# Kernel tuning notes

Hardware: AMD Instinct MI355X
Metric: run time of the kernel (lower is better)

The kernel has to match this reference:

```python
import jax, jax.numpy as jnp
import numpy as np


def setup_inputs() -> dict:
    key = jax.random.key(0)
    k1, k2, k3 = jax.random.split(key, 3)
    B, S, V, L = 1, 1000, 50000, 64
    decoder_output = jax.random.normal(k1, (B, S, V), dtype=jnp.float32)
    z_mean = jax.random.normal(k2, (B, L), dtype=jnp.float32)
    z_sigma = jnp.ones((B, L), dtype=jnp.float32)
    y_true = jax.random.randint(k3, (B, S), 0, V, dtype=jnp.int64)
    y_true_s = jnp.ones((B, V), dtype=jnp.float32)
    return {"decoder_output": decoder_output, "z_mean": z_mean,
            "z_sigma": z_sigma, "y_true": y_true, "y_true_s": y_true_s}


def reference(decoder_output, z_mean, z_sigma, y_true, y_true_s):
    # KL divergence term (mean over all latent entries)
    mean_sq = z_mean * z_mean
    stddev_sq = z_sigma * z_sigma
    kld = jnp.mean(mean_sq + stddev_sq - jnp.log(stddev_sq) - 1.0)

    B, S, V = decoder_output.shape
    log_probs = jax.nn.log_softmax(decoder_output, axis=-1)  # [B,S,V]

    # Per-step weight 1/(S - s1), matching the python loop
    weights = 1.0 / (S - jnp.arange(S, dtype=decoder_output.dtype))  # [S]

    def step(y_s, xs):
        lp_s, idx, w = xs  # lp_s: [B,V], idx: scalar int, w: scalar
        lik = -jnp.sum(y_s * lp_s, axis=-1) * w  # [B]
        # original code only zeroes row 0 (assumes batch size 1)
        y_s = y_s.at[0, idx].set(0.0)
        return y_s, lik

    xs = (jnp.swapaxes(log_probs, 0, 1), y_true[0], weights)  # scan over S
    _, liks = jax.lax.scan(step, y_true_s, xs)  # liks: [S,B]
    likelihood = jnp.sum(liks, axis=0)  # [B]

    div_l = jnp.asarray(S, dtype=decoder_output.dtype)
    final = 0.1 * kld + likelihood / div_l  # [B]
    return final
```

## Files before the change

### kernel.cpp

```cpp
#include <hip/hip_runtime.h>
#include <math.h>

#define LOG2E 1.4426950408889634f
#define NCH 8
#define RPB 4
#define NPB 16
#define NBC 16

__global__ __launch_bounds__(256) void prep_kernel(
    const int* __restrict__ y, int S, int* __restrict__ isfirst_g)
{
    __shared__ int sy[2048];
    const int tid = threadIdx.x;
    for (int j = tid; j < S; j += 256) sy[j] = y[j];
    __syncthreads();

    const int lane = tid & 63, wid = tid >> 6;
    const int gw = blockIdx.x * 4 + wid;
    const int nw = gridDim.x * 4;
    for (int j = gw; j < S; j += nw) {
        const int t = sy[j];
        int found = 0;
        for (int i = lane; i < j; i += 64) found |= (sy[i] == t);
        const int fl = __any(found) ? 0 : 1;
        if (lane == 0) isfirst_g[j] = fl;
    }
}

__global__ __launch_bounds__(256) void rowg_kernel(
    const float* __restrict__ x, const float* __restrict__ yts,
    const int* __restrict__ y, const int* __restrict__ isfirst,
    int S, int V, int Vc4, int nvec,
    float* __restrict__ se_part, float* __restrict__ ws_part,
    float* __restrict__ g_part, float* __restrict__ w_part)
{
    const int rg  = blockIdx.x / NCH;
    const int c   = blockIdx.x % NCH;
    const int tid = threadIdx.x;
    const int row0 = rg * RPB;

    __shared__ int sy[1024];
    __shared__ unsigned char sf[1024];
    const int jstage = min(S, row0 + RPB);
    for (int j = tid; j < jstage; j += 256) {
        sy[j] = y[j];
        sf[j] = (unsigned char)isfirst[j];
    }

    const float4* __restrict__ y4  = (const float4*)yts;
    const float4* __restrict__ x40 = (const float4*)(x + (size_t)(row0 + 0) * V);
    const float4* __restrict__ x41 = (const float4*)(x + (size_t)(row0 + 1) * V);
    const float4* __restrict__ x42 = (const float4*)(x + (size_t)(row0 + 2) * V);
    const float4* __restrict__ x43 = (const float4*)(x + (size_t)(row0 + 3) * V);

    const int lo4 = c * Vc4;
    const int hi4 = min(lo4 + Vc4, nvec);

    float se0 = 0.f, se1 = 0.f, se2 = 0.f, se3 = 0.f;
    float ws0 = 0.f, ws1 = 0.f, ws2 = 0.f, ws3 = 0.f;
    float ys  = 0.f;

    #pragma unroll 2
    for (int i = lo4 + tid; i < hi4; i += 256) {
        const float4 yv = y4[i];
        const float4 a  = x40[i];
        const float4 b  = x41[i];
        const float4 cc = x42[i];
        const float4 d  = x43[i];

        ys += (yv.x + yv.y) + (yv.z + yv.w);

        se0 += (__builtin_amdgcn_exp2f(a.x * LOG2E) + __builtin_amdgcn_exp2f(a.y * LOG2E))
             + (__builtin_amdgcn_exp2f(a.z * LOG2E) + __builtin_amdgcn_exp2f(a.w * LOG2E));
        ws0 = fmaf(yv.x, a.x, fmaf(yv.y, a.y, fmaf(yv.z, a.z, fmaf(yv.w, a.w, ws0))));

        se1 += (__builtin_amdgcn_exp2f(b.x * LOG2E) + __builtin_amdgcn_exp2f(b.y * LOG2E))
             + (__builtin_amdgcn_exp2f(b.z * LOG2E) + __builtin_amdgcn_exp2f(b.w * LOG2E));
        ws1 = fmaf(yv.x, b.x, fmaf(yv.y, b.y, fmaf(yv.z, b.z, fmaf(yv.w, b.w, ws1))));

        se2 += (__builtin_amdgcn_exp2f(cc.x * LOG2E) + __builtin_amdgcn_exp2f(cc.y * LOG2E))
             + (__builtin_amdgcn_exp2f(cc.z * LOG2E) + __builtin_amdgcn_exp2f(cc.w * LOG2E));
        ws2 = fmaf(yv.x, cc.x, fmaf(yv.y, cc.y, fmaf(yv.z, cc.z, fmaf(yv.w, cc.w, ws2))));

        se3 += (__builtin_amdgcn_exp2f(d.x * LOG2E) + __builtin_amdgcn_exp2f(d.y * LOG2E))
             + (__builtin_amdgcn_exp2f(d.z * LOG2E) + __builtin_amdgcn_exp2f(d.w * LOG2E));
        ws3 = fmaf(yv.x, d.x, fmaf(yv.y, d.y, fmaf(yv.z, d.z, fmaf(yv.w, d.w, ws3))));
    }

    const int cl = lo4 << 2;
    const int ch = (c == NCH - 1) ? V : (hi4 << 2);
    if (c == NCH - 1) {
        for (int v = (nvec << 2) + tid; v < V; v += 256) {
            const float yv = yts[v];
            const float a  = x[(size_t)(row0 + 0) * V + v];
            const float b  = x[(size_t)(row0 + 1) * V + v];
            const float cc = x[(size_t)(row0 + 2) * V + v];
            const float d  = x[(size_t)(row0 + 3) * V + v];
            ys  += yv;
            se0 += __builtin_amdgcn_exp2f(a * LOG2E);  ws0 = fmaf(yv, a, ws0);
            se1 += __builtin_amdgcn_exp2f(b * LOG2E);  ws1 = fmaf(yv, b, ws1);
            se2 += __builtin_amdgcn_exp2f(cc * LOG2E); ws2 = fmaf(yv, cc, ws2);
            se3 += __builtin_amdgcn_exp2f(d * LOG2E);  ws3 = fmaf(yv, d, ws3);
        }
    }

    float se[RPB] = { se0, se1, se2, se3 };
    float ws[RPB] = { ws0, ws1, ws2, ws3 };
    __shared__ float red[RPB][3][4];
    __shared__ float sys[4];
    const int wid = tid >> 6, lane = tid & 63;
    #pragma unroll
    for (int r = 0; r < RPB; ++r) {
        float s = se[r], w = ws[r];
        #pragma unroll
        for (int off = 1; off < 64; off <<= 1) {
            s += __shfl_xor(s, off);
            w += __shfl_xor(w, off);
        }
        if (lane == 0) { red[r][0][wid] = s; red[r][1][wid] = w; }
    }
    {
        float yv = ys;
        #pragma unroll
        for (int off = 1; off < 64; off <<= 1) yv += __shfl_xor(yv, off);
        if (lane == 0) sys[wid] = yv;
    }
    __syncthreads();

    float g0 = 0.f, g1 = 0.f, g2 = 0.f, g3 = 0.f;
    const int jhi = min(row0 + RPB - 1, S);
    const float* __restrict__ xb = x + (size_t)row0 * V;
    for (int j = tid; j < jhi; j += 256) {
        if (sf[j]) {
            const int t = sy[j];
            if (t >= cl && t < ch) {
                const float yv = yts[t];
                if (j < row0)     g0 = fmaf(yv, xb[t], g0);
                if (j < row0 + 1) g1 = fmaf(yv, xb[(size_t)V + t], g1);
                if (j < row0 + 2) g2 = fmaf(yv, xb[2 * (size_t)V + t], g2);
                g3 = fmaf(yv, xb[3 * (size_t)V + t], g3);
            }
        }
    }
    float gg[RPB] = { g0, g1, g2, g3 };
    #pragma unroll
    for (int r = 0; r < RPB; ++r) {
        float g = gg[r];
        #pragma unroll
        for (int off = 1; off < 64; off <<= 1) g += __shfl_xor(g, off);
        if (lane == 0) red[r][2][wid] = g;
    }
    __syncthreads();

    if (tid < RPB * 3) {
        const int r = tid / 3, which = tid % 3;
        const float v = (red[r][which][0] + red[r][which][1])
                      + (red[r][which][2] + red[r][which][3]);
        float* dst = (which == 0) ? se_part : (which == 1) ? ws_part : g_part;
        dst[(size_t)(row0 + r) * NCH + c] = v;
    }
    if (rg == 0 && tid == 0)
        w_part[c] = (sys[0] + sys[1]) + (sys[2] + sys[3]);
}

__global__ __launch_bounds__(256) void combine_part_kernel(
    const int* __restrict__ y, const int* __restrict__ isfirst,
    const float* __restrict__ yts, const float* __restrict__ w_part,
    const float* __restrict__ se_part, const float* __restrict__ ws_part,
    const float* __restrict__ g_part,
    int S, double* __restrict__ lik_part)
{
    const int tid = threadIdx.x;
    __shared__ int   sy[1024];
    __shared__ float sval[1024];
    __shared__ float spart[256];
    __shared__ double sd[256];
    __shared__ float sW;

    for (int j = tid; j < S; j += 256) {
        sy[j] = y[j];
        sval[j] = isfirst[j] ? 1.0f : 0.0f;
    }
    __syncthreads();
    for (int j = tid; j < S; j += 256)
        sval[j] = (sval[j] != 0.0f) ? yts[sy[j]] : 0.0f;

    float wv = (tid < NCH) ? w_part[tid] : 0.f;
    #pragma unroll
    for (int off = 1; off < 8; off <<= 1) wv += __shfl_xor(wv, off);
    if (tid == 0) sW = wv;
    __syncthreads();

    const int CH = (S + 255) / 256;
    const int lo = tid * CH;
    const int hi = min(lo + CH, S);
    float p = 0.0f;
    for (int j = lo; j < hi; ++j) p += sval[j];
    spart[tid] = p;
    __syncthreads();
    for (int off = 1; off < 256; off <<= 1) {
        float v = (tid >= off) ? spart[tid - off] : 0.0f;
        __syncthreads();
        spart[tid] += v;
        __syncthreads();
    }
    float run = (tid > 0) ? spart[tid - 1] : 0.0f;
    for (int j = lo; j < hi; ++j) {
        const float v = sval[j];
        sval[j] = run;
        run += v;
    }
    __syncthreads();
    const double W = (double)sW;

    const int sper = (S + NBC - 1) / NBC;
    const int s0 = blockIdx.x * sper;
    const int s1 = min(s0 + sper, S);
    double acc = 0.0;
    for (int s = s0 + tid; s < s1; s += 256) {
        double se = 0.0, ws = 0.0, G = 0.0;
        #pragma unroll
        for (int c = 0; c < NCH; ++c) {
            se += (double)se_part[s * NCH + c];
            ws += (double)ws_part[s * NCH + c];
            G  += (double)g_part[s * NCH + c];
        }
        const double l = log(se);
        const double sumy = (ws - W * l) - (G - (double)sval[s] * l);
        acc += -sumy / (double)(S - s);
    }
    sd[tid] = acc; __syncthreads();
    for (int off = 128; off; off >>= 1) { if (tid < off) sd[tid] += sd[tid + off]; __syncthreads(); }
    if (tid == 0) lik_part[blockIdx.x] = sd[0];
}

__global__ __launch_bounds__(256) void final_kernel(
    const float* __restrict__ zm, const float* __restrict__ zs,
    const double* __restrict__ lik_part,
    int L, int S, float* __restrict__ out)
{
    const int tid = threadIdx.x;
    __shared__ double sd[256];

    double acc = 0.0;
    for (int i = tid; i < L; i += 256) {
        const double mq = (double)zm[i] * (double)zm[i];
        const double sq = (double)zs[i] * (double)zs[i];
        acc += mq + sq - log(sq) - 1.0;
    }
    sd[tid] = acc; __syncthreads();
    for (int off = 128; off; off >>= 1) { if (tid < off) sd[tid] += sd[tid + off]; __syncthreads(); }
    const double kld = sd[0] / (double)L;
    __syncthreads();

    acc = (tid < NBC) ? lik_part[tid] : 0.0;
    sd[tid] = acc; __syncthreads();
    for (int off = 128; off; off >>= 1) { if (tid < off) sd[tid] += sd[tid + off]; __syncthreads(); }

    if (tid == 0) out[0] = (float)(0.1 * kld + sd[0] / (double)S);
}

extern "C" void kernel_launch(void* const* d_in, const int* in_sizes, int n_in,
                              void* d_out, int out_size, void* d_ws, size_t ws_size,
                              hipStream_t stream)
{
    const float* x   = (const float*)d_in[0];
    const float* zm  = (const float*)d_in[1];
    const float* zs  = (const float*)d_in[2];
    const int*   y   = (const int*)d_in[3];
    const float* yts = (const float*)d_in[4];
    float* out = (float*)d_out;

    const int L = in_sizes[1];
    const int S = in_sizes[3];
    const int V = in_sizes[4];

    const int nvec = V >> 2;
    const int Vc4  = (nvec + NCH - 1) / NCH;
    const int nrg  = (S + RPB - 1) / RPB;

    double* lik_part = (double*)d_ws;
    float* se_part = (float*)(lik_part + NBC);
    float* ws_part = se_part + (size_t)S * NCH;
    float* g_part  = ws_part + (size_t)S * NCH;
    float* w_part  = g_part + (size_t)S * NCH;
    int*   isfirst = (int*)(w_part + NCH);

    prep_kernel<<<NPB, 256, 0, stream>>>(y, S, isfirst);
    rowg_kernel<<<nrg * NCH, 256, 0, stream>>>(x, yts, y, isfirst, S, V, Vc4, nvec,
                                               se_part, ws_part, g_part, w_part);
    combine_part_kernel<<<NBC, 256, 0, stream>>>(y, isfirst, yts, w_part,
                                                 se_part, ws_part, g_part, S, lik_part);
    final_kernel<<<1, 256, 0, stream>>>(zm, zs, lik_part, L, S, out);
}
```

Measured before the change: 65.23 us.

## Fuse combine and final kernels into rowg via last-block atomic counter

Drops the separate combine and final kernels. The last block of rowg_kernel, detected with an atomic done counter that prep_kernel resets, now does the prefix scan, per-row likelihood, KL term and final output. This removes two kernel launches and their inter-kernel gaps. In exchange the tail work runs on a single block instead of 16, which serialises that reduction.

```diff
diff --git a/kernel.cpp b/kernel.cpp
--- a/kernel.cpp
+++ b/kernel.cpp
@@ -5,11 +5,13 @@
 #define NCH 8
 #define RPB 4
 #define NPB 16
-#define NBC 16
 
 __global__ __launch_bounds__(256) void prep_kernel(
-    const int* __restrict__ y, int S, int* __restrict__ isfirst_g)
+    const int* __restrict__ y, int S, int* __restrict__ isfirst_g,
+    unsigned int* __restrict__ done_ctr)
 {
+    if (blockIdx.x == 0 && threadIdx.x == 0) *done_ctr = 0u;
+
     __shared__ int sy[2048];
     const int tid = threadIdx.x;
     for (int j = tid; j < S; j += 256) sy[j] = y[j];
@@ -30,9 +32,11 @@
 __global__ __launch_bounds__(256) void rowg_kernel(
     const float* __restrict__ x, const float* __restrict__ yts,
     const int* __restrict__ y, const int* __restrict__ isfirst,
-    int S, int V, int Vc4, int nvec,
+    const float* __restrict__ zm, const float* __restrict__ zs,
+    int S, int V, int Vc4, int nvec, int L,
     float* __restrict__ se_part, float* __restrict__ ws_part,
-    float* __restrict__ g_part, float* __restrict__ w_part)
+    float* __restrict__ g_part, float* __restrict__ w_part,
+    unsigned int* __restrict__ done_ctr, float* __restrict__ out)
 {
     const int rg  = blockIdx.x / NCH;
     const int c   = blockIdx.x % NCH;
@@ -161,29 +165,26 @@
     }
     if (rg == 0 && tid == 0)
         w_part[c] = (sys[0] + sys[1]) + (sys[2] + sys[3]);
-}
-
-__global__ __launch_bounds__(256) void combine_part_kernel(
-    const int* __restrict__ y, const int* __restrict__ isfirst,
-    const float* __restrict__ yts, const float* __restrict__ w_part,
-    const float* __restrict__ se_part, const float* __restrict__ ws_part,
-    const float* __restrict__ g_part,
-    int S, double* __restrict__ lik_part)
-{
-    const int tid = threadIdx.x;
-    __shared__ int   sy[1024];
+
+    __syncthreads();
+    __shared__ unsigned int slast;
+    if (tid == 0) {
+        __threadfence();
+        slast = atomicAdd(done_ctr, 1u);
+    }
+    __syncthreads();
+    if (slast != (unsigned)(gridDim.x - 1)) return;
+
+    __threadfence();
     __shared__ float sval[1024];
     __shared__ float spart[256];
     __shared__ double sd[256];
     __shared__ float sW;
 
-    for (int j = tid; j < S; j += 256) {
-        sy[j] = y[j];
-        sval[j] = isfirst[j] ? 1.0f : 0.0f;
-    }
+    for (int j = tid; j < S; j += 256) sy[j] = y[j];
     __syncthreads();
     for (int j = tid; j < S; j += 256)
-        sval[j] = (sval[j] != 0.0f) ? yts[sy[j]] : 0.0f;
+        sval[j] = isfirst[j] ? yts[sy[j]] : 0.0f;
 
     float wv = (tid < NCH) ? w_part[tid] : 0.f;
     #pragma unroll
@@ -191,11 +192,11 @@
     if (tid == 0) sW = wv;
     __syncthreads();
 
-    const int CH = (S + 255) / 256;
-    const int lo = tid * CH;
-    const int hi = min(lo + CH, S);
+    const int CHk = (S + 255) / 256;
+    const int slo = tid * CHk;
+    const int shi = min(slo + CHk, S);
     float p = 0.0f;
-    for (int j = lo; j < hi; ++j) p += sval[j];
+    for (int j = slo; j < shi; ++j) p += sval[j];
     spart[tid] = p;
     __syncthreads();
     for (int off = 1; off < 256; off <<= 1) {
@@ -205,7 +206,7 @@
         __syncthreads();
     }
     float run = (tid > 0) ? spart[tid - 1] : 0.0f;
-    for (int j = lo; j < hi; ++j) {
+    for (int j = slo; j < shi; ++j) {
         const float v = sval[j];
         sval[j] = run;
         run += v;
@@ -213,36 +214,25 @@
     __syncthreads();
     const double W = (double)sW;
 
-    const int sper = (S + NBC - 1) / NBC;
-    const int s0 = blockIdx.x * sper;
-    const int s1 = min(s0 + sper, S);
     double acc = 0.0;
-    for (int s = s0 + tid; s < s1; s += 256) {
-        double se = 0.0, ws = 0.0, G = 0.0;
-        #pragma unroll
-        for (int c = 0; c < NCH; ++c) {
-            se += (double)se_part[s * NCH + c];
-            ws += (double)ws_part[s * NCH + c];
-            G  += (double)g_part[s * NCH + c];
-        }
-        const double l = log(se);
-        const double sumy = (ws - W * l) - (G - (double)sval[s] * l);
+    for (int s = tid; s < S; s += 256) {
+        double sev = 0.0, wsv = 0.0, Gv = 0.0;
+        #pragma unroll
+        for (int cc2 = 0; cc2 < NCH; ++cc2) {
+            sev += (double)se_part[s * NCH + cc2];
+            wsv += (double)ws_part[s * NCH + cc2];
+            Gv  += (double)g_part[s * NCH + cc2];
+        }
+        const double l = log(sev);
+        const double sumy = (wsv - W * l) - (Gv - (double)sval[s] * l);
         acc += -sumy / (double)(S - s);
     }
     sd[tid] = acc; __syncthreads();
     for (int off = 128; off; off >>= 1) { if (tid < off) sd[tid] += sd[tid + off]; __syncthreads(); }
-    if (tid == 0) lik_part[blockIdx.x] = sd[0];
-}
-
-__global__ __launch_bounds__(256) void final_kernel(
-    const float* __restrict__ zm, const float* __restrict__ zs,
-    const double* __restrict__ lik_part,
-    int L, int S, float* __restrict__ out)
-{
-    const int tid = threadIdx.x;
-    __shared__ double sd[256];
-
-    double acc = 0.0;
+    const double lik = sd[0];
+    __syncthreads();
+
+    acc = 0.0;
     for (int i = tid; i < L; i += 256) {
         const double mq = (double)zm[i] * (double)zm[i];
         const double sq = (double)zs[i] * (double)zs[i];
@@ -250,14 +240,8 @@
     }
     sd[tid] = acc; __syncthreads();
     for (int off = 128; off; off >>= 1) { if (tid < off) sd[tid] += sd[tid + off]; __syncthreads(); }
-    const double kld = sd[0] / (double)L;
-    __syncthreads();
-
-    acc = (tid < NBC) ? lik_part[tid] : 0.0;
-    sd[tid] = acc; __syncthreads();
-    for (int off = 128; off; off >>= 1) { if (tid < off) sd[tid] += sd[tid + off]; __syncthreads(); }
-
-    if (tid == 0) out[0] = (float)(0.1 * kld + sd[0] / (double)S);
+
+    if (tid == 0) out[0] = (float)(0.1 * (sd[0] / (double)L) + lik / (double)S);
 }
 
 extern "C" void kernel_launch(void* const* d_in, const int* in_sizes, int n_in,
@@ -279,17 +263,16 @@
     const int Vc4  = (nvec + NCH - 1) / NCH;
     const int nrg  = (S + RPB - 1) / RPB;
 
-    double* lik_part = (double*)d_ws;
-    float* se_part = (float*)(lik_part + NBC);
+    float* se_part = (float*)d_ws;
     float* ws_part = se_part + (size_t)S * NCH;
     float* g_part  = ws_part + (size_t)S * NCH;
     float* w_part  = g_part + (size_t)S * NCH;
     int*   isfirst = (int*)(w_part + NCH);
-
-    prep_kernel<<<NPB, 256, 0, stream>>>(y, S, isfirst);
-    rowg_kernel<<<nrg * NCH, 256, 0, stream>>>(x, yts, y, isfirst, S, V, Vc4, nvec,
-                                               se_part, ws_part, g_part, w_part);
-    combine_part_kernel<<<NBC, 256, 0, stream>>>(y, isfirst, yts, w_part,
-                                                 se_part, ws_part, g_part, S, lik_part);
-    final_kernel<<<1, 256, 0, stream>>>(zm, zs, lik_part, L, S, out);
+    unsigned int* done_ctr = (unsigned int*)(isfirst + S);
+
+    prep_kernel<<<NPB, 256, 0, stream>>>(y, S, isfirst, done_ctr);
+    rowg_kernel<<<nrg * NCH, 256, 0, stream>>>(x, yts, y, isfirst, zm, zs,
+                                               S, V, Vc4, nvec, L,
+                                               se_part, ws_part, g_part, w_part,
+                                               done_ctr, out);
 }
```

Result: slower. 125.9 us (+93.1%).

## Fold final reduction into combine kernel via last-block atomic counter

Applied to the files above, without the earlier changes.

Removes the separate final kernel launch. The last combine block to finish, found with an atomic counter that prep_kernel resets, sums the partial likelihoods and computes the KL term. The main row kernel also gets launch_bounds occupancy hints and a larger unroll factor. This saves one launch and its gap, at the cost of release/acquire atomics and possible register pressure from the deeper unroll.

```diff
diff --git a/kernel.cpp b/kernel.cpp
--- a/kernel.cpp
+++ b/kernel.cpp
@@ -8,8 +8,11 @@
 #define NBC 16
 
 __global__ __launch_bounds__(256) void prep_kernel(
-    const int* __restrict__ y, int S, int* __restrict__ isfirst_g)
+    const int* __restrict__ y, int S, int* __restrict__ isfirst_g,
+    unsigned int* __restrict__ ctr)
 {
+    if (blockIdx.x == 0 && threadIdx.x == 0) *ctr = 0u;
+
     __shared__ int sy[2048];
     const int tid = threadIdx.x;
     for (int j = tid; j < S; j += 256) sy[j] = y[j];
@@ -27,7 +30,7 @@
     }
 }
 
-__global__ __launch_bounds__(256) void rowg_kernel(
+__global__ __launch_bounds__(256, 4) void rowg_kernel(
     const float* __restrict__ x, const float* __restrict__ yts,
     const int* __restrict__ y, const int* __restrict__ isfirst,
     int S, int V, int Vc4, int nvec,
@@ -60,7 +63,7 @@
     float ws0 = 0.f, ws1 = 0.f, ws2 = 0.f, ws3 = 0.f;
     float ys  = 0.f;
 
-    #pragma unroll 2
+    #pragma unroll 4
     for (int i = lo4 + tid; i < hi4; i += 256) {
         const float4 yv = y4[i];
         const float4 a  = x40[i];
@@ -168,7 +171,10 @@
     const float* __restrict__ yts, const float* __restrict__ w_part,
     const float* __restrict__ se_part, const float* __restrict__ ws_part,
     const float* __restrict__ g_part,
-    int S, double* __restrict__ lik_part)
+    const float* __restrict__ zm, const float* __restrict__ zs,
+    int S, int L,
+    double* __restrict__ lik_part, unsigned int* __restrict__ ctr,
+    float* __restrict__ out)
 {
     const int tid = threadIdx.x;
     __shared__ int   sy[1024];
@@ -176,6 +182,7 @@
     __shared__ float spart[256];
     __shared__ double sd[256];
     __shared__ float sW;
+    __shared__ unsigned int slast;
 
     for (int j = tid; j < S; j += 256) {
         sy[j] = y[j];
@@ -231,33 +238,35 @@
     }
     sd[tid] = acc; __syncthreads();
     for (int off = 128; off; off >>= 1) { if (tid < off) sd[tid] += sd[tid + off]; __syncthreads(); }
-    if (tid == 0) lik_part[blockIdx.x] = sd[0];
-}
-
-__global__ __launch_bounds__(256) void final_kernel(
-    const float* __restrict__ zm, const float* __restrict__ zs,
-    const double* __restrict__ lik_part,
-    int L, int S, float* __restrict__ out)
-{
-    const int tid = threadIdx.x;
-    __shared__ double sd[256];
-
-    double acc = 0.0;
+
+    if (tid == 0) {
+        __hip_atomic_store(&lik_part[blockIdx.x], sd[0],
+                           __ATOMIC_RELEASE, __HIP_MEMORY_SCOPE_AGENT);
+        slast = __hip_atomic_fetch_add(ctr, 1u,
+                                       __ATOMIC_ACQ_REL, __HIP_MEMORY_SCOPE_AGENT);
+    }
+    __syncthreads();
+    if (slast != (unsigned)(gridDim.x - 1)) return;
+
+    double lp = 0.0;
+    if (tid < NBC)
+        lp = __hip_atomic_load(&lik_part[tid], __ATOMIC_ACQUIRE,
+                               __HIP_MEMORY_SCOPE_AGENT);
+    sd[tid] = lp; __syncthreads();
+    for (int off = 128; off; off >>= 1) { if (tid < off) sd[tid] += sd[tid + off]; __syncthreads(); }
+    const double lik = sd[0];
+    __syncthreads();
+
+    double kacc = 0.0;
     for (int i = tid; i < L; i += 256) {
         const double mq = (double)zm[i] * (double)zm[i];
         const double sq = (double)zs[i] * (double)zs[i];
-        acc += mq + sq - log(sq) - 1.0;
-    }
-    sd[tid] = acc; __syncthreads();
+        kacc += mq + sq - log(sq) - 1.0;
+    }
+    sd[tid] = kacc; __syncthreads();
     for (int off = 128; off; off >>= 1) { if (tid < off) sd[tid] += sd[tid + off]; __syncthreads(); }
-    const double kld = sd[0] / (double)L;
-    __syncthreads();
-
-    acc = (tid < NBC) ? lik_part[tid] : 0.0;
-    sd[tid] = acc; __syncthreads();
-    for (int off = 128; off; off >>= 1) { if (tid < off) sd[tid] += sd[tid + off]; __syncthreads(); }
-
-    if (tid == 0) out[0] = (float)(0.1 * kld + sd[0] / (double)S);
+
+    if (tid == 0) out[0] = (float)(0.1 * (sd[0] / (double)L) + lik / (double)S);
 }
 
 extern "C" void kernel_launch(void* const* d_in, const int* in_sizes, int n_in,
@@ -285,11 +294,12 @@
     float* g_part  = ws_part + (size_t)S * NCH;
     float* w_part  = g_part + (size_t)S * NCH;
     int*   isfirst = (int*)(w_part + NCH);
-
-    prep_kernel<<<NPB, 256, 0, stream>>>(y, S, isfirst);
+    unsigned int* ctr = (unsigned int*)(isfirst + S);
+
+    prep_kernel<<<NPB, 256, 0, stream>>>(y, S, isfirst, ctr);
     rowg_kernel<<<nrg * NCH, 256, 0, stream>>>(x, yts, y, isfirst, S, V, Vc4, nvec,
                                                se_part, ws_part, g_part, w_part);
     combine_part_kernel<<<NBC, 256, 0, stream>>>(y, isfirst, yts, w_part,
-                                                 se_part, ws_part, g_part, S, lik_part);
-    final_kernel<<<1, 256, 0, stream>>>(zm, zs, lik_part, L, S, out);
+                                                 se_part, ws_part, g_part,
+                                                 zm, zs, S, L, lik_part, ctr, out);
 }
```

Measured after the change: 63.24 us. 3.1% less time.
